# Kernel optimization log

Measured on AMD Instinct MI355X. Metric: run time of the kernel, lower is better.

## Reference

```python
import jax, jax.numpy as jnp
import numpy as np

B, D, T = 8, 256, 4096      # batch, latent dim, frames
NQ, K = 8, 1024             # num quantizers, codebook size


def setup_inputs() -> dict:
    key = jax.random.key(0)
    k1, k2 = jax.random.split(key)
    x = jax.random.normal(k1, (B, D, T), dtype=jnp.float32)
    codebooks = jax.random.normal(k2, (NQ, K, D), dtype=jnp.float32)
    return {"x": x, "codebooks": codebooks}


def _vq(residual, cb):
    """Single VQ stage: nearest-neighbor in cb, lookup, VQ loss.
    residual: [B, T, D], cb: [K, D]
    """
    sg = jax.lax.stop_gradient
    dots = jnp.einsum('btd,kd->btk', residual, cb)                 # [B,T,K]
    dist = (residual ** 2).sum(-1, keepdims=True) - 2.0 * dots + (cb ** 2).sum(-1)
    idx = jnp.argmin(dist, axis=-1)                                # [B,T]
    q = cb[idx]                                                    # gather [B,T,D]
    # commitment loss + codebook loss (standard VQ-VAE combination)
    loss = jnp.mean((sg(q) - residual) ** 2) + jnp.mean((q - sg(residual)) ** 2)
    return q, idx, loss


def reference(x, codebooks):
    """Residual VQ forward (eval mode, train=False).
    x: [B, D, T]; codebooks: [NQ, K, D]
    Returns (quantized_out [B,T,D], indices [NQ,B,T], losses [NQ]).
    """
    residual0 = jnp.transpose(x, (0, 2, 1))                        # [B,T,D]

    def step(carry, cb):
        res, qout = carry
        q, idx, loss = _vq(res, cb)
        q = jax.lax.stop_gradient(q)
        return (res - q, qout + q), (idx, loss)

    (_, quantized_out), (indices, losses) = jax.lax.scan(
        step, (residual0, jnp.zeros_like(residual0)), codebooks)
    return quantized_out, indices, losses
```

## Files before the change

### kernel.cpp

```cpp
#include <hip/hip_runtime.h>

#define B_   8
#define D_   256
#define T_   4096
#define NQ_  8
#define K_   1024

#define IDX_OFF  ((size_t)B_ * T_ * D_)
#define LOSS_OFF (IDX_OFF + (size_t)NQ_ * B_ * T_)

#define XT_OFF   0ull
#define CB16_OFF 33554432ull
#define CN_OFF   37748736ull
#define LB_OFF   37781504ull

typedef _Float16 half8 __attribute__((ext_vector_type(8)));
typedef float   f32x16 __attribute__((ext_vector_type(16)));

__device__ __forceinline__ ushort f2h(float f) {
  return __builtin_bit_cast(ushort, (_Float16)f);
}

__device__ __forceinline__ float packsc(float sc, uint code) {
  return __builtin_bit_cast(float, (__builtin_bit_cast(uint, sc) & ~1023u) | code);
}
__device__ __forceinline__ void ins3(float& v1, float& v2, float& v3, float f) {
  const float a = v1;
  const float m = fmaxf(v1, f);
  v1 = fminf(v1, f);
  const float v2n = __builtin_amdgcn_fmed3f(a, v2, f);
  v3 = __builtin_amdgcn_fmed3f(v2, v3, m);
  v2 = v2n;
}

__global__ void prep_xT(const float* __restrict__ x, float* __restrict__ xT) {
  __shared__ float tile[64][65];
  const int bidx = blockIdx.x;
  const int b = bidx >> 8, dc = (bidx >> 6) & 3, tc = bidx & 63;
  const int d0 = dc * 64, t0 = tc * 64;
  const int tid = threadIdx.x;
  {
    const int tt = tid & 63, dg = tid >> 6;
    for (int i = 0; i < 16; ++i) {
      const int d = dg * 16 + i;
      tile[d][tt] = x[((size_t)(b * D_ + d0 + d)) * T_ + t0 + tt];
    }
  }
  __syncthreads();
  {
    const int dw = tid & 63, tg = tid >> 6;
    for (int i = 0; i < 16; ++i) {
      const int t = tg * 16 + i;
      xT[((size_t)b * T_ + t0 + t) * D_ + d0 + dw] = tile[dw][t];
    }
  }
}

__global__ void prep_cb16(const float* __restrict__ cb, ushort* __restrict__ cb16,
                          float* __restrict__ cnorm) {
  const int tid = threadIdx.x, w = tid >> 6, l = tid & 63;
  const int code = blockIdx.x * 4 + w;
  const int s = code >> 10, ci = code & 1023, tile = ci >> 5, n = ci & 31;
  const float* row = cb + (size_t)code * D_;
  const float4 v = *(const float4*)(row + l * 4);
  double nrm = (double)v.x * v.x + (double)v.y * v.y + (double)v.z * v.z + (double)v.w * v.w;
  ushort4 p;
  p.x = f2h(v.x); p.y = f2h(v.y); p.z = f2h(v.z); p.w = f2h(v.w);
  const int ks = l >> 2, lf = ((l >> 1) & 1) * 32 + n, j0 = (l & 1) * 4;
  const size_t off = (((size_t)s * 32 + tile) * 16 + ks) * 512 + (size_t)lf * 8 + j0;
  *(ushort4*)(cb16 + off) = p;
#pragma unroll
  for (int m = 1; m <= 32; m <<= 1) nrm += __shfl_xor(nrm, m);
  if (l == 0) cnorm[code] = (float)nrm;
}

__global__ __launch_bounds__(512)
void rvq_main(const float* __restrict__ cb, const float* __restrict__ xT,
              const ushort* __restrict__ cb16, const float* __restrict__ cnorm,
              float* __restrict__ out, double* __restrict__ lossbuf) {
  __shared__ __align__(16) uint4  res16[2048];
  __shared__ float candm[64][12];

  const int tid = threadIdx.x;
  const int w = tid >> 6, l = tid & 63, n5 = l & 31, h = l >> 5;
  const int g = w >> 2, ww = w & 3;
  const size_t row0 = (size_t)blockIdx.x * 64;
  const int rowL = tid >> 3;
  const int g3 = rowL >> 5;
  const int dq = tid & 7;

  float res[4][8];

  {
#pragma unroll
    for (int cc = 0; cc < 4; ++cc) {
      const int kb = dq * 4 + cc;
      const float* xp = xT + (row0 + rowL) * D_ + kb * 8;
      const float4 x0 = *(const float4*)xp, x1 = *(const float4*)(xp + 4);
      res[cc][0] = x0.x; res[cc][1] = x0.y; res[cc][2] = x0.z; res[cc][3] = x0.w;
      res[cc][4] = x1.x; res[cc][5] = x1.y; res[cc][6] = x1.z; res[cc][7] = x1.w;
      uint4 pv;
      pv.x = __builtin_bit_cast(uint, __builtin_amdgcn_cvt_pkrtz(x0.x, x0.y));
      pv.y = __builtin_bit_cast(uint, __builtin_amdgcn_cvt_pkrtz(x0.z, x0.w));
      pv.z = __builtin_bit_cast(uint, __builtin_amdgcn_cvt_pkrtz(x1.x, x1.y));
      pv.w = __builtin_bit_cast(uint, __builtin_amdgcn_cvt_pkrtz(x1.z, x1.w));
      res16[g3 * 1024 + kb * 32 + ((rowL & 31) ^ dq)] = pv;
    }
  }
  __syncthreads();

  for (int s = 0; s < NQ_; ++s) {
    float v1 = 3e38f, v2 = 3e38f, v3 = 3e38f;
    float u1 = 3e38f, u2 = 3e38f, u3 = 3e38f;
    for (int tt = 0; tt < 8; ++tt) {
      const int t = ww * 8 + tt;
      const uint4* ap = (const uint4*)(cb16 + ((size_t)(s * 32 + t) * 16) * 512) + l;
      int zr = 0;
      asm volatile("" : "+v"(zr));
      const uint4* bp = res16 + g * 1024 + zr;
      f32x16 acc;
#pragma unroll
      for (int r = 0; r < 16; ++r) acc[r] = 0.0f;
#pragma unroll
      for (int q = 0; q < 4; ++q) {
        uint4 av[4], bv[4];
#pragma unroll
        for (int c = 0; c < 4; ++c) {
          const int ks = q * 4 + c;
          av[c] = ap[(size_t)ks * 64];
          bv[c] = bp[(ks * 2 + h) * 32 + (n5 ^ ((ks >> 1) & 7))];
        }
#pragma unroll
        for (int c = 0; c < 4; ++c) {
          acc = __builtin_amdgcn_mfma_f32_32x32x16_f16(
              __builtin_bit_cast(half8, av[c]), __builtin_bit_cast(half8, bv[c]), acc, 0, 0, 0);
        }
      }
      const float* cnb = cnorm + s * K_ + t * 32 + h * 4;
      const uint cbase = (uint)(t * 32 + 4 * h);
#pragma unroll
      for (int q = 0; q < 4; ++q) {
        const float4 cq = *(const float4*)(cnb + q * 8);
        const float cna[4] = {cq.x, cq.y, cq.z, cq.w};
#pragma unroll
        for (int rr = 0; rr < 4; ++rr) {
          const int r = q * 4 + rr;
          const float sc = cna[rr] - 2.0f * acc[r];
          const uint code = cbase + (uint)(8 * q + rr);
          const float f = packsc(sc, code);
          if (rr & 1) ins3(u1, u2, u3, f);
          else        ins3(v1, v2, v3, f);
        }
      }
    }
    ins3(v1, v2, v3, u1);
    ins3(v1, v2, v3, u2);
    ins3(v1, v2, v3, u3);
    {
      const float o1 = __shfl_xor(v1, 32), o2 = __shfl_xor(v2, 32), o3 = __shfl_xor(v3, 32);
      ins3(v1, v2, v3, o1);
      ins3(v1, v2, v3, o2);
      ins3(v1, v2, v3, o3);
    }
    if (h == 0) {
      candm[g * 32 + n5][ww * 3 + 0] = v1;
      candm[g * 32 + n5][ww * 3 + 1] = v2;
      candm[g * 32 + n5][ww * 3 + 2] = v3;
    }
    __syncthreads();

    double lossW = 0.0;
    {
      float m1 = 3e38f, m2 = 3e38f, m3 = 3e38f;
#pragma unroll
      for (int cd = 0; cd < 12; ++cd) ins3(m1, m2, m3, candm[rowL][cd]);
      const int c1 = (int)(__builtin_bit_cast(uint, m1) & 1023u);
      const int c2 = (int)(__builtin_bit_cast(uint, m2) & 1023u);
      const int c3 = (int)(__builtin_bit_cast(uint, m3) & 1023u);

      const float* cbs = cb + (size_t)s * K_ * D_;
      const float* cr0 = cbs + (size_t)c1 * D_;
      const float* cr1 = cbs + (size_t)c2 * D_;
      const float* cr2 = cbs + (size_t)c3 * D_;
      double dd0 = 0.0, dd1 = 0.0, dd2 = 0.0;
#pragma unroll
      for (int cc = 0; cc < 4; ++cc) {
        const int kb = dq * 4 + cc;
        const int go = kb * 8;
        const float4 a0 = *(const float4*)(cr0 + go), a1 = *(const float4*)(cr0 + go + 4);
        const float4 b0 = *(const float4*)(cr1 + go), b1 = *(const float4*)(cr1 + go + 4);
        const float4 g0 = *(const float4*)(cr2 + go), g1 = *(const float4*)(cr2 + go + 4);
        const float af[8] = {a0.x, a0.y, a0.z, a0.w, a1.x, a1.y, a1.z, a1.w};
        const float bf[8] = {b0.x, b0.y, b0.z, b0.w, b1.x, b1.y, b1.z, b1.w};
        const float gf[8] = {g0.x, g0.y, g0.z, g0.w, g1.x, g1.y, g1.z, g1.w};
#pragma unroll
        for (int j = 0; j < 8; ++j) {
          const double r64 = (double)res[cc][j];
          const double u = r64 - (double)af[j]; dd0 += u * u;
          const double v = r64 - (double)bf[j]; dd1 += v * v;
          const double gg = r64 - (double)gf[j]; dd2 += gg * gg;
        }
      }
#pragma unroll
      for (int m = 1; m <= 4; m <<= 1) {
        dd0 += __shfl_xor(dd0, m); dd1 += __shfl_xor(dd1, m); dd2 += __shfl_xor(dd2, m);
      }
      int win = c1; double dwn = dd0;
      if (dd1 < dwn || (dd1 == dwn && c2 < win)) { win = c2; dwn = dd1; }
      if (dd2 < dwn || (dd2 == dwn && c3 < win)) { win = c3; dwn = dd2; }
      const float* crw = cbs + (size_t)win * D_;
#pragma unroll
      for (int cc = 0; cc < 4; ++cc) {
        const int kb = dq * 4 + cc;
        const int go = kb * 8;
        const float4 w0 = *(const float4*)(crw + go), w1 = *(const float4*)(crw + go + 4);
        const float wf[8] = {w0.x, w0.y, w0.z, w0.w, w1.x, w1.y, w1.z, w1.w};
        if (s < NQ_ - 1) {
#pragma unroll
          for (int j = 0; j < 8; ++j) res[cc][j] = res[cc][j] - wf[j];
          uint4 pv;
          pv.x = __builtin_bit_cast(uint, __builtin_amdgcn_cvt_pkrtz(res[cc][0], res[cc][1]));
          pv.y = __builtin_bit_cast(uint, __builtin_amdgcn_cvt_pkrtz(res[cc][2], res[cc][3]));
          pv.z = __builtin_bit_cast(uint, __builtin_amdgcn_cvt_pkrtz(res[cc][4], res[cc][5]));
          pv.w = __builtin_bit_cast(uint, __builtin_amdgcn_cvt_pkrtz(res[cc][6], res[cc][7]));
          res16[g3 * 1024 + kb * 32 + ((rowL & 31) ^ dq)] = pv;
        } else {
          const float* xp = xT + (row0 + rowL) * D_ + go;
          const float4 x0 = *(const float4*)xp, x1 = *(const float4*)(xp + 4);
          const float xf[8] = {x0.x, x0.y, x0.z, x0.w, x1.x, x1.y, x1.z, x1.w};
          float o[8];
#pragma unroll
          for (int j = 0; j < 8; ++j) o[j] = xf[j] - (res[cc][j] - wf[j]);
          float* od = out + (row0 + rowL) * D_ + go;
          *(float4*)od       = make_float4(o[0], o[1], o[2], o[3]);
          *(float4*)(od + 4) = make_float4(o[4], o[5], o[6], o[7]);
        }
      }
      if (dq == 0) {
        out[IDX_OFF + (size_t)s * (B_ * T_) + row0 + rowL] = (float)win;
        lossW = dwn;
      }
    }
#pragma unroll
    for (int m = 8; m <= 32; m <<= 1) lossW += __shfl_xor(lossW, m);
    if (l == 0) atomicAdd(&lossbuf[s], lossW);
    __syncthreads();
  }
}

__global__ void rvq_loss(const double* __restrict__ lossbuf, float* __restrict__ out) {
  const int s = threadIdx.x;
  if (s < NQ_) out[LOSS_OFF + s] = (float)(2.0 * lossbuf[s] / (double)((size_t)B_ * T_ * D_));
}

extern "C" void kernel_launch(void* const* d_in, const int* in_sizes, int n_in,
                              void* d_out, int out_size, void* d_ws, size_t ws_size,
                              hipStream_t stream) {
  const float* x  = (const float*)d_in[0];
  const float* cb = (const float*)d_in[1];
  float* out = (float*)d_out;
  char* ws = (char*)d_ws;
  float*  xTp   = (float*)(ws + XT_OFF);
  ushort* cb16p = (ushort*)(ws + CB16_OFF);
  float*  cnp   = (float*)(ws + CN_OFF);
  double* lbp   = (double*)(ws + LB_OFF);

  hipMemsetAsync(ws + LB_OFF, 0, NQ_ * sizeof(double), stream);
  prep_xT<<<2048, 256, 0, stream>>>(x, xTp);
  prep_cb16<<<2048, 256, 0, stream>>>(cb, cb16p, cnp);
  rvq_main<<<512, 512, 0, stream>>>(cb, xTp, cb16p, cnp, out, lbp);
  rvq_loss<<<1, 64, 0, stream>>>(lbp, out);
}
```

Measured before the change: 571.3 us.

## Halve block size, reuse each codebook A-fragment across two row groups

```diff
diff --git a/kernel.cpp b/kernel.cpp
--- a/kernel.cpp
+++ b/kernel.cpp
@@ -74,106 +74,112 @@
   if (l == 0) cnorm[code] = (float)nrm;
 }
 
-__global__ __launch_bounds__(512)
+__global__ __launch_bounds__(256)
 void rvq_main(const float* __restrict__ cb, const float* __restrict__ xT,
               const ushort* __restrict__ cb16, const float* __restrict__ cnorm,
               float* __restrict__ out, double* __restrict__ lossbuf) {
   __shared__ __align__(16) uint4  res16[2048];
   __shared__ float candm[64][12];
+  __shared__ double lred[4];
 
   const int tid = threadIdx.x;
   const int w = tid >> 6, l = tid & 63, n5 = l & 31, h = l >> 5;
-  const int g = w >> 2, ww = w & 3;
   const size_t row0 = (size_t)blockIdx.x * 64;
-  const int rowL = tid >> 3;
-  const int g3 = rowL >> 5;
+  const int rowL31 = tid >> 3;
   const int dq = tid & 7;
 
-  float res[4][8];
-
-  {
+  float res[2][4][8];
+
+#pragma unroll
+  for (int g3 = 0; g3 < 2; ++g3) {
 #pragma unroll
     for (int cc = 0; cc < 4; ++cc) {
       const int kb = dq * 4 + cc;
-      const float* xp = xT + (row0 + rowL) * D_ + kb * 8;
+      const float* xp = xT + (row0 + g3 * 32 + rowL31) * D_ + kb * 8;
       const float4 x0 = *(const float4*)xp, x1 = *(const float4*)(xp + 4);
-      res[cc][0] = x0.x; res[cc][1] = x0.y; res[cc][2] = x0.z; res[cc][3] = x0.w;
-      res[cc][4] = x1.x; res[cc][5] = x1.y; res[cc][6] = x1.z; res[cc][7] = x1.w;
+      res[g3][cc][0] = x0.x; res[g3][cc][1] = x0.y; res[g3][cc][2] = x0.z; res[g3][cc][3] = x0.w;
+      res[g3][cc][4] = x1.x; res[g3][cc][5] = x1.y; res[g3][cc][6] = x1.z; res[g3][cc][7] = x1.w;
       uint4 pv;
       pv.x = __builtin_bit_cast(uint, __builtin_amdgcn_cvt_pkrtz(x0.x, x0.y));
       pv.y = __builtin_bit_cast(uint, __builtin_amdgcn_cvt_pkrtz(x0.z, x0.w));
       pv.z = __builtin_bit_cast(uint, __builtin_amdgcn_cvt_pkrtz(x1.x, x1.y));
       pv.w = __builtin_bit_cast(uint, __builtin_amdgcn_cvt_pkrtz(x1.z, x1.w));
-      res16[g3 * 1024 + kb * 32 + ((rowL & 31) ^ dq)] = pv;
+      res16[g3 * 1024 + kb * 32 + (rowL31 ^ dq)] = pv;
     }
   }
   __syncthreads();
 
   for (int s = 0; s < NQ_; ++s) {
-    float v1 = 3e38f, v2 = 3e38f, v3 = 3e38f;
-    float u1 = 3e38f, u2 = 3e38f, u3 = 3e38f;
+    float a1v = 3e38f, a2v = 3e38f, a3v = 3e38f;
+    float b1v = 3e38f, b2v = 3e38f, b3v = 3e38f;
+    float c1v = 3e38f, c2v = 3e38f, c3v = 3e38f;
+    float d1v = 3e38f, d2v = 3e38f, d3v = 3e38f;
     for (int tt = 0; tt < 8; ++tt) {
-      const int t = ww * 8 + tt;
+      const int t = w * 8 + tt;
       const uint4* ap = (const uint4*)(cb16 + ((size_t)(s * 32 + t) * 16) * 512) + l;
       int zr = 0;
       asm volatile("" : "+v"(zr));
-      const uint4* bp = res16 + g * 1024 + zr;
-      f32x16 acc;
-#pragma unroll
-      for (int r = 0; r < 16; ++r) acc[r] = 0.0f;
+      const uint4* bp = res16 + zr;
+      f32x16 acc0, acc1;
+#pragma unroll
+      for (int r = 0; r < 16; ++r) { acc0[r] = 0.0f; acc1[r] = 0.0f; }
 #pragma unroll
       for (int q = 0; q < 4; ++q) {
-        uint4 av[4], bv[4];
+        uint4 av[4], b0[4], b1[4];
 #pragma unroll
         for (int c = 0; c < 4; ++c) {
           const int ks = q * 4 + c;
+          const int bo = (ks * 2 + h) * 32 + (n5 ^ ((ks >> 1) & 7));
           av[c] = ap[(size_t)ks * 64];
-          bv[c] = bp[(ks * 2 + h) * 32 + (n5 ^ ((ks >> 1) & 7))];
+          b0[c] = bp[bo];
+          b1[c] = bp[1024 + bo];
         }
 #pragma unroll
         for (int c = 0; c < 4; ++c) {
-          acc = __builtin_amdgcn_mfma_f32_32x32x16_f16(
-              __builtin_bit_cast(half8, av[c]), __builtin_bit_cast(half8, bv[c]), acc, 0, 0, 0);
+          acc0 = __builtin_amdgcn_mfma_f32_32x32x16_f16(
+              __builtin_bit_cast(half8, av[c]), __builtin_bit_cast(half8, b0[c]), acc0, 0, 0, 0);
+          acc1 = __builtin_amdgcn_mfma_f32_32x32x16_f16(
+              __builtin_bit_cast(half8, av[c]), __builtin_bit_cast(half8, b1[c]), acc1, 0, 0, 0);
         }
       }
       const float* cnb = cnorm + s * K_ + t * 32 + h * 4;
       const uint cbase = (uint)(t * 32 + 4 * h);
 #pragma unroll
-      for (int q = 0; q < 4; ++q) {
-        const float4 cq = *(const float4*)(cnb + q * 8);
+      for (int qq = 0; qq < 4; ++qq) {
+        const float4 cq = *(const float4*)(cnb + qq * 8);
         const float cna[4] = {cq.x, cq.y, cq.z, cq.w};
 #pragma unroll
         for (int rr = 0; rr < 4; ++rr) {
-          const int r = q * 4 + rr;
-          const float sc = cna[rr] - 2.0f * acc[r];
-          const uint code = cbase + (uint)(8 * q + rr);
-          const float f = packsc(sc, code);
-          if (rr & 1) ins3(u1, u2, u3, f);
-          else        ins3(v1, v2, v3, f);
-        }
-      }
-    }
-    ins3(v1, v2, v3, u1);
-    ins3(v1, v2, v3, u2);
-    ins3(v1, v2, v3, u3);
+          const int r = qq * 4 + rr;
+          const uint code = cbase + (uint)(8 * qq + rr);
+          const float f0 = packsc(fmaf(-2.0f, acc0[r], cna[rr]), code);
+          const float f1 = packsc(fmaf(-2.0f, acc1[r], cna[rr]), code);
+          if (rr & 1) { ins3(b1v, b2v, b3v, f0); ins3(d1v, d2v, d3v, f1); }
+          else        { ins3(a1v, a2v, a3v, f0); ins3(c1v, c2v, c3v, f1); }
+        }
+      }
+    }
+    ins3(a1v, a2v, a3v, b1v); ins3(a1v, a2v, a3v, b2v); ins3(a1v, a2v, a3v, b3v);
+    ins3(c1v, c2v, c3v, d1v); ins3(c1v, c2v, c3v, d2v); ins3(c1v, c2v, c3v, d3v);
     {
-      const float o1 = __shfl_xor(v1, 32), o2 = __shfl_xor(v2, 32), o3 = __shfl_xor(v3, 32);
-      ins3(v1, v2, v3, o1);
-      ins3(v1, v2, v3, o2);
-      ins3(v1, v2, v3, o3);
+      const float o1 = __shfl_xor(a1v, 32), o2 = __shfl_xor(a2v, 32), o3 = __shfl_xor(a3v, 32);
+      ins3(a1v, a2v, a3v, o1); ins3(a1v, a2v, a3v, o2); ins3(a1v, a2v, a3v, o3);
+      const float p1 = __shfl_xor(c1v, 32), p2 = __shfl_xor(c2v, 32), p3 = __shfl_xor(c3v, 32);
+      ins3(c1v, c2v, c3v, p1); ins3(c1v, c2v, c3v, p2); ins3(c1v, c2v, c3v, p3);
     }
     if (h == 0) {
-      candm[g * 32 + n5][ww * 3 + 0] = v1;
-      candm[g * 32 + n5][ww * 3 + 1] = v2;
-      candm[g * 32 + n5][ww * 3 + 2] = v3;
+      candm[n5][w * 3 + 0] = a1v; candm[n5][w * 3 + 1] = a2v; candm[n5][w * 3 + 2] = a3v;
+      candm[32 + n5][w * 3 + 0] = c1v; candm[32 + n5][w * 3 + 1] = c2v; candm[32 + n5][w * 3 + 2] = c3v;
     }
     __syncthreads();
 
     double lossW = 0.0;
-    {
+#pragma unroll
+    for (int g3 = 0; g3 < 2; ++g3) {
+      const int row = g3 * 32 + rowL31;
       float m1 = 3e38f, m2 = 3e38f, m3 = 3e38f;
 #pragma unroll
-      for (int cd = 0; cd < 12; ++cd) ins3(m1, m2, m3, candm[rowL][cd]);
+      for (int cd = 0; cd < 12; ++cd) ins3(m1, m2, m3, candm[row][cd]);
       const int c1 = (int)(__builtin_bit_cast(uint, m1) & 1023u);
       const int c2 = (int)(__builtin_bit_cast(uint, m2) & 1023u);
       const int c3 = (int)(__builtin_bit_cast(uint, m3) & 1023u);
@@ -195,7 +201,7 @@
         const float gf[8] = {g0.x, g0.y, g0.z, g0.w, g1.x, g1.y, g1.z, g1.w};
 #pragma unroll
         for (int j = 0; j < 8; ++j) {
-          const double r64 = (double)res[cc][j];
+          const double r64 = (double)res[g3][cc][j];
           const double u = r64 - (double)af[j]; dd0 += u * u;
           const double v = r64 - (double)bf[j]; dd1 += v * v;
           const double gg = r64 - (double)gf[j]; dd2 += gg * gg;
@@ -217,40 +223,50 @@
         const float wf[8] = {w0.x, w0.y, w0.z, w0.w, w1.x, w1.y, w1.z, w1.w};
         if (s < NQ_ - 1) {
 #pragma unroll
-          for (int j = 0; j < 8; ++j) res[cc][j] = res[cc][j] - wf[j];
+          for (int j = 0; j < 8; ++j) res[g3][cc][j] = res[g3][cc][j] - wf[j];
           uint4 pv;
-          pv.x = __builtin_bit_cast(uint, __builtin_amdgcn_cvt_pkrtz(res[cc][0], res[cc][1]));
-          pv.y = __builtin_bit_cast(uint, __builtin_amdgcn_cvt_pkrtz(res[cc][2], res[cc][3]));
-          pv.z = __builtin_bit_cast(uint, __builtin_amdgcn_cvt_pkrtz(res[cc][4], res[cc][5]));
-          pv.w = __builtin_bit_cast(uint, __builtin_amdgcn_cvt_pkrtz(res[cc][6], res[cc][7]));
-          res16[g3 * 1024 + kb * 32 + ((rowL & 31) ^ dq)] = pv;
+          pv.x = __builtin_bit_cast(uint, __builtin_amdgcn_cvt_pkrtz(res[g3][cc][0], res[g3][cc][1]));
+          pv.y = __builtin_bit_cast(uint, __builtin_amdgcn_cvt_pkrtz(res[g3][cc][2], res[g3][cc][3]));
+          pv.z = __builtin_bit_cast(uint, __builtin_amdgcn_cvt_pkrtz(res[g3][cc][4], res[g3][cc][5]));
+          pv.w = __builtin_bit_cast(uint, __builtin_amdgcn_cvt_pkrtz(res[g3][cc][6], res[g3][cc][7]));
+          res16[g3 * 1024 + kb * 32 + (rowL31 ^ dq)] = pv;
         } else {
-          const float* xp = xT + (row0 + rowL) * D_ + go;
+          const float* xp = xT + (row0 + row) * D_ + go;
           const float4 x0 = *(const float4*)xp, x1 = *(const float4*)(xp + 4);
           const float xf[8] = {x0.x, x0.y, x0.z, x0.w, x1.x, x1.y, x1.z, x1.w};
           float o[8];
 #pragma unroll
-          for (int j = 0; j < 8; ++j) o[j] = xf[j] - (res[cc][j] - wf[j]);
-          float* od = out + (row0 + rowL) * D_ + go;
+          for (int j = 0; j < 8; ++j) o[j] = xf[j] - (res[g3][cc][j] - wf[j]);
+          float* od = out + (row0 + row) * D_ + go;
           *(float4*)od       = make_float4(o[0], o[1], o[2], o[3]);
           *(float4*)(od + 4) = make_float4(o[4], o[5], o[6], o[7]);
         }
       }
       if (dq == 0) {
-        out[IDX_OFF + (size_t)s * (B_ * T_) + row0 + rowL] = (float)win;
-        lossW = dwn;
+        out[IDX_OFF + (size_t)s * (B_ * T_) + row0 + row] = (float)win;
+        lossW += dwn;
       }
     }
 #pragma unroll
     for (int m = 8; m <= 32; m <<= 1) lossW += __shfl_xor(lossW, m);
-    if (l == 0) atomicAdd(&lossbuf[s], lossW);
+    if (l == 0) lred[w] = lossW;
     __syncthreads();
+    if (tid == 0)
+      lossbuf[(size_t)s * 512 + blockIdx.x] = lred[0] + lred[1] + lred[2] + lred[3];
   }
 }
 
 __global__ void rvq_loss(const double* __restrict__ lossbuf, float* __restrict__ out) {
-  const int s = threadIdx.x;
-  if (s < NQ_) out[LOSS_OFF + s] = (float)(2.0 * lossbuf[s] / (double)((size_t)B_ * T_ * D_));
+  const int s = blockIdx.x, tid = threadIdx.x;
+  double acc = lossbuf[(size_t)s * 512 + tid] + lossbuf[(size_t)s * 512 + tid + 256];
+#pragma unroll
+  for (int m = 1; m <= 32; m <<= 1) acc += __shfl_xor(acc, m);
+  __shared__ double sred[4];
+  if ((tid & 63) == 0) sred[tid >> 6] = acc;
+  __syncthreads();
+  if (tid == 0)
+    out[LOSS_OFF + s] =
+        (float)(2.0 * (sred[0] + sred[1] + sred[2] + sred[3]) / (double)((size_t)B_ * T_ * D_));
 }
 
 extern "C" void kernel_launch(void* const* d_in, const int* in_sizes, int n_in,
@@ -265,9 +281,8 @@
   float*  cnp   = (float*)(ws + CN_OFF);
   double* lbp   = (double*)(ws + LB_OFF);
 
-  hipMemsetAsync(ws + LB_OFF, 0, NQ_ * sizeof(double), stream);
   prep_xT<<<2048, 256, 0, stream>>>(x, xTp);
   prep_cb16<<<2048, 256, 0, stream>>>(cb, cb16p, cnp);
-  rvq_main<<<512, 512, 0, stream>>>(cb, xTp, cb16p, cnp, out, lbp);
-  rvq_loss<<<1, 64, 0, stream>>>(lbp, out);
-}
+  rvq_main<<<512, 256, 0, stream>>>(cb, xTp, cb16p, cnp, out, lbp);
+  rvq_loss<<<8, 256, 0, stream>>>(lbp, out);
+}
```

Result: faster. 490.3 us (-14.2%).
